# Optimization experiments

Measured on AMD Instinct MI355X. Metric: run time of the kernel, lower is better.

Reference implementation:

```python
import jax, jax.numpy as jnp
import numpy as np

B, T, D, H = 32, 512, 512, 8
DH = D // H  # 64


def _pos_enc(t, d):
    # pos / 10000^(2i/d) for ALL i, then sin on even cols, cos on odd cols, scaled by sqrt(d)
    pos = np.arange(t, dtype=np.float64)[:, None]
    i = np.arange(d, dtype=np.float64)[None, :]
    ang = pos / np.power(10000.0, 2.0 * i / d)
    pe = np.empty((t, d), dtype=np.float64)
    pe[:, 0::2] = np.sin(ang[:, 0::2])
    pe[:, 1::2] = np.cos(ang[:, 1::2])
    return jnp.asarray(pe * np.sqrt(float(d)), dtype=jnp.float32)


def setup_inputs() -> dict:
    key = jax.random.key(0)
    ks = jax.random.split(key, 9)
    return {
        "queries": jax.random.normal(ks[0], (B, T, D), dtype=jnp.float32),
        "keys": jax.random.normal(ks[1], (B, T, D), dtype=jnp.float32),
        "query_masks": jax.random.randint(ks[2], (B,), 0, T, dtype=jnp.int32),
        "key_masks": jax.random.randint(ks[3], (B,), 0, T, dtype=jnp.int32),
        "W_Q": jax.random.normal(ks[4], (D, D), dtype=jnp.float32) * 0.05,
        "W_K": jax.random.normal(ks[5], (D, D), dtype=jnp.float32) * 0.05,
        "W_V": jax.random.normal(ks[6], (D, D), dtype=jnp.float32) * 0.05,
        "fw1": jax.random.normal(ks[7], (D, 4 * D), dtype=jnp.float32) * 0.05,
        "fw2": jax.random.normal(ks[8], (4 * D, D), dtype=jnp.float32) * 0.05,
    }


def reference(queries, keys, query_masks, key_masks, W_Q, W_K, W_V, fw1, fw2):
    pe = _pos_enc(T, D)  # [T, D]
    # Source bug kept: queries = posenc(queries); keys = posenc(queries)  -> keys input unused
    q1 = queries + pe[None]          # [B,T,D]
    k1 = q1 + pe[None]               # pos-encoded twice
    Q = q1 @ W_Q                     # [B,T,D]
    Kp = k1 @ W_K                    # [B,T,D]
    V = Kp @ W_V                     # source bug kept: values from projected keys
    # split heads (head-major fold in the original concat(split) idiom)
    Qh = Q.reshape(B, T, H, DH).transpose(2, 0, 1, 3)   # [H,B,T,dh]
    Kh = Kp.reshape(B, T, H, DH).transpose(2, 0, 1, 3)
    Vh = V.reshape(B, T, H, DH).transpose(2, 0, 1, 3)
    scores = jnp.einsum('hbqd,hbkd->hbqk', Qh, Kh) / jnp.sqrt(jnp.float32(DH))
    # source subtracts max over the QUERY axis (axis=1 of [H*B,T,T]) = axis 2 here
    scores = scores - scores.max(axis=2, keepdims=True)
    attn = jax.nn.softmax(scores, axis=-1)
    qmask = (jnp.arange(T)[None, :] < query_masks[:, None]).astype(jnp.float32)  # [B,T]
    attn = attn * qmask[None, :, :, None]
    out = jnp.einsum('hbqk,hbkd->hbqd', attn, Vh)       # [H,B,T,dh]
    result = out.transpose(1, 2, 0, 3).reshape(B, T, D) + q1  # residual with pos-encoded queries
    hidden = jax.nn.relu(result @ fw1)                  # [B,T,4D]
    result = result + hidden @ fw2                      # residual; no layer norm (use_layer_norm=False)
    return result
```

## Files before the change

kernel.cpp:

```cpp
#include <hip/hip_runtime.h>
#include <cstdint>
#include <cstddef>

typedef __bf16 bf16x8 __attribute__((ext_vector_type(8)));
typedef float f32x4 __attribute__((ext_vector_type(4)));
using u16 = unsigned short;
using u32 = unsigned int;

__device__ __forceinline__ u16 f2b(float f) {
  u32 u = __float_as_uint(f);
  u32 r = u + 0x7FFFu + ((u >> 16) & 1u);
  return (u16)(r >> 16);
}
__device__ __forceinline__ float b2f(u16 h) { return __uint_as_float((u32)h << 16); }

__device__ __forceinline__ void gload16(const void* g, void* l) {
  __builtin_amdgcn_global_load_lds((const __attribute__((address_space(1))) void*)g,
                                   (__attribute__((address_space(3))) void*)l, 16, 0, 0);
}

__device__ __forceinline__ u32 mapf(float f) {
  u32 u = __float_as_uint(f);
  return (u & 0x80000000u) ? ~u : (u | 0x80000000u);
}
__device__ __forceinline__ float unmapf(u32 k) {
  u32 u = (k & 0x80000000u) ? (k ^ 0x80000000u) : ~k;
  return __uint_as_float(u);
}
__device__ __forceinline__ u32 cvtpk(float lo, float hi) {
  u32 r;
  asm("v_cvt_pk_bf16_f32 %0, %1, %2" : "=v"(r) : "v"(lo), "v"(hi));
  return r;
}

#define MFMA __builtin_amdgcn_mfma_f32_16x16x32_bf16

__global__ void pe_kernel(float* __restrict__ pe) {
  int i = blockIdx.x * 256 + threadIdx.x;
  if (i >= 512 * 512) return;
  int t = i >> 9, d = i & 511;
  double ang = (double)t * exp((double)d * (-2.0 / 512.0) * log(10000.0));
  double v = (d & 1) ? cos(ang) : sin(ang);
  pe[i] = (float)(v * 22.627416997969522);
}

__global__ void wconv_kernel(const float* __restrict__ WQ, const float* __restrict__ WK,
                             const float* __restrict__ WV, const float* __restrict__ f1,
                             const float* __restrict__ f2,
                             u16* __restrict__ WQth, u16* __restrict__ WQtl,
                             u16* __restrict__ WKth, u16* __restrict__ WKtl,
                             u16* __restrict__ WKb, u16* __restrict__ WVt,
                             u16* __restrict__ f1t, u16* __restrict__ f2t) {
  int i = blockIdx.x * 256 + threadIdx.x;
  if (i < 262144) {
    int n = i >> 9, k = i & 511;
    float wq = WQ[k * 512 + n];
    u16 h = f2b(wq);
    WQth[i] = h;
    WQtl[i] = f2b(wq - b2f(h));
    float wk = WK[k * 512 + n];
    h = f2b(wk);
    WKth[i] = h;
    WKtl[i] = f2b(wk - b2f(h));
    WKb[i] = f2b(WK[i]);
    WVt[i] = f2b(WV[k * 512 + n]);
  } else if (i < 262144 + 1048576) {
    int i2 = i - 262144;
    int n = i2 >> 9, k = i2 & 511;
    f1t[i2] = f2b(f1[k * 2048 + n]);
  } else if (i < 262144 + 2097152) {
    int i3 = i - 262144 - 1048576;
    int n = i3 >> 11, k = i3 & 2047;
    f2t[i3] = f2b(f2[k * 512 + n]);
  }
}

__global__ void prep_kernel(const float* __restrict__ q, const float* __restrict__ pe,
                            u16* __restrict__ q1h, u16* __restrict__ q1l,
                            u16* __restrict__ k1h, u16* __restrict__ k1l,
                            u32* __restrict__ m0) {
  int i = blockIdx.x * 256 + threadIdx.x;
  if (i < 131072) m0[i] = 0u;
  if (i >= 32 * 512 * 512) return;
  int td = i & (262144 - 1);
  float p = pe[td];
  float q1 = q[i] + p;
  float k1 = q1 + p;
  u16 h = f2b(q1);
  q1h[i] = h;
  q1l[i] = f2b(q1 - b2f(h));
  h = f2b(k1);
  k1h[i] = h;
  k1l[i] = f2b(k1 - b2f(h));
}

#define GM_BF16 0
#define GM_RELU 2
#define GM_ADDF32 3

template <int MODE>
__global__ __launch_bounds__(256, 2) void gemm_bt(const u16* __restrict__ A,
                                                  const u16* __restrict__ B, int M, int N, int K,
                                                  u16* __restrict__ outb, float* __restrict__ outf,
                                                  const float* __restrict__ res) {
  __shared__ u16 As[128 * 32];
  __shared__ u16 Bs[128 * 32];
  const int tid = threadIdx.x, lane = tid & 63, w = tid >> 6;
  const int wm = w >> 1, wn = w & 1;
  const long aBase = (long)blockIdx.x * 128;
  const long bBase = (long)blockIdx.y * 128;
  f32x4 acc[4][4] = {};
  const int nk = K >> 5;
  for (int kt = 0; kt < nk; ++kt) {
#pragma unroll
    for (int i = 0; i < 2; ++i) {
      const int c = w * 2 + i;
      const int off = c * 1024 + lane * 16;
      const int r = off >> 6, cb = off & 63;
      gload16((const char*)A + ((aBase + r) * (long)K + (long)kt * 32) * 2 + cb,
              (char*)As + c * 1024);
      gload16((const char*)B + ((bBase + r) * (long)K + (long)kt * 32) * 2 + cb,
              (char*)Bs + c * 1024);
    }
    __syncthreads();
    bf16x8 af[4], bfr[4];
#pragma unroll
    for (int x = 0; x < 4; ++x) {
      af[x] = *(const bf16x8*)&As[(wm * 64 + x * 16 + (lane & 15)) * 32 + (lane >> 4) * 8];
      bfr[x] = *(const bf16x8*)&Bs[(wn * 64 + x * 16 + (lane & 15)) * 32 + (lane >> 4) * 8];
    }
#pragma unroll
    for (int mf = 0; mf < 4; ++mf)
#pragma unroll
      for (int nf = 0; nf < 4; ++nf)
        acc[mf][nf] = MFMA(af[mf], bfr[nf], acc[mf][nf], 0, 0, 0);
    __syncthreads();
  }
#pragma unroll
  for (int mf = 0; mf < 4; ++mf)
#pragma unroll
    for (int nf = 0; nf < 4; ++nf) {
      const long row0 = aBase + wm * 64 + mf * 16 + (lane >> 4) * 4;
      const long col = bBase + wn * 64 + nf * 16 + (lane & 15);
#pragma unroll
      for (int j = 0; j < 4; ++j) {
        float v = acc[mf][nf][j];
        const long row = row0 + j;
        if (MODE == GM_BF16)
          outb[row * N + col] = f2b(v);
        else if (MODE == GM_RELU)
          outb[row * N + col] = f2b(v > 0.f ? v : 0.f);
        else
          outf[row * N + col] = res[row * N + col] + v;
      }
    }
}

__global__ __launch_bounds__(256, 2) void gemm_split(const u16* __restrict__ Ah,
                                                     const u16* __restrict__ Al,
                                                     const u16* __restrict__ Bh,
                                                     const u16* __restrict__ Bl, int M, int N,
                                                     int K, u16* __restrict__ Oh,
                                                     u16* __restrict__ Ol) {
  __shared__ u16 Ash[4096], Asl[4096], Bsh[4096], Bsl[4096];
  const int tid = threadIdx.x, lane = tid & 63, w = tid >> 6;
  const int wm = w >> 1, wn = w & 1;
  const long aBase = (long)blockIdx.x * 128;
  const long bBase = (long)blockIdx.y * 128;
  f32x4 acc[4][4] = {};
  const int nk = K >> 5;
  for (int kt = 0; kt < nk; ++kt) {
#pragma unroll
    for (int i = 0; i < 2; ++i) {
      const int c = w * 2 + i;
      const int off = c * 1024 + lane * 16;
      const int r = off >> 6, cb = off & 63;
      long ga = ((aBase + r) * (long)K + (long)kt * 32) * 2 + cb;
      long gb = ((bBase + r) * (long)K + (long)kt * 32) * 2 + cb;
      gload16((const char*)Ah + ga, (char*)Ash + c * 1024);
      gload16((const char*)Al + ga, (char*)Asl + c * 1024);
      gload16((const char*)Bh + gb, (char*)Bsh + c * 1024);
      gload16((const char*)Bl + gb, (char*)Bsl + c * 1024);
    }
    __syncthreads();
    bf16x8 ah[4], al[4], bh[4], bl[4];
#pragma unroll
    for (int x = 0; x < 4; ++x) {
      int ao = (wm * 64 + x * 16 + (lane & 15)) * 32 + (lane >> 4) * 8;
      int bo = (wn * 64 + x * 16 + (lane & 15)) * 32 + (lane >> 4) * 8;
      ah[x] = *(const bf16x8*)&Ash[ao];
      al[x] = *(const bf16x8*)&Asl[ao];
      bh[x] = *(const bf16x8*)&Bsh[bo];
      bl[x] = *(const bf16x8*)&Bsl[bo];
    }
#pragma unroll
    for (int mf = 0; mf < 4; ++mf)
#pragma unroll
      for (int nf = 0; nf < 4; ++nf) {
        acc[mf][nf] = MFMA(ah[mf], bh[nf], acc[mf][nf], 0, 0, 0);
        acc[mf][nf] = MFMA(ah[mf], bl[nf], acc[mf][nf], 0, 0, 0);
        acc[mf][nf] = MFMA(al[mf], bh[nf], acc[mf][nf], 0, 0, 0);
      }
    __syncthreads();
  }
#pragma unroll
  for (int mf = 0; mf < 4; ++mf)
#pragma unroll
    for (int nf = 0; nf < 4; ++nf) {
      const long row0 = aBase + wm * 64 + mf * 16 + (lane >> 4) * 4;
      const long col = bBase + wn * 64 + nf * 16 + (lane & 15);
#pragma unroll
      for (int j = 0; j < 4; ++j) {
        float v = acc[mf][nf][j];
        const long row = row0 + j;
        u16 h = f2b(v);
        Oh[row * N + col] = h;
        Ol[row * N + col] = f2b(v - b2f(h));
      }
    }
}

__global__ __launch_bounds__(256, 4) void attn_colmax(const u16* __restrict__ Qh,
                                                      const u16* __restrict__ Ql,
                                                      const u16* __restrict__ Kh,
                                                      const u16* __restrict__ Kl,
                                                      u32* __restrict__ mg) {
  __shared__ u16 Qsh[4096], Qsl[4096];
  __shared__ u16 Ksh[4096], Ksl[4096];
  __shared__ u32 mloc[512];
  const int tid = threadIdx.x, lane = tid & 63, w = tid >> 6;
  const int ql = lane & 15, g = lane >> 4;
  const int hb = blockIdx.x, b = hb >> 3, h = hb & 7, qc = blockIdx.y;
  mloc[tid] = 0u;
  mloc[tid + 256] = 0u;
  const int srccb = 16 * ((lane & 7) ^ ((lane >> 3) & 7));
#pragma unroll
  for (int i = 0; i < 2; ++i) {
    const int c = w * 2 + i;
    const int r = c * 8 + (lane >> 3);
    long gb = ((long)(b * 512 + qc * 64 + r) * 512 + h * 64) * 2 + srccb;
    gload16((const char*)Qh + gb, (char*)Qsh + c * 1024);
    gload16((const char*)Ql + gb, (char*)Qsl + c * 1024);
  }
  __syncthreads();
  const int qrow = w * 16 + ql;
  const int sw0 = ((g * 16) ^ ((ql & 7) * 16)) >> 1;
  const int sw1 = ((64 + g * 16) ^ ((ql & 7) * 16)) >> 1;
  bf16x8 qh0 = *(const bf16x8*)&Qsh[qrow * 64 + sw0];
  bf16x8 ql0 = *(const bf16x8*)&Qsl[qrow * 64 + sw0];
  bf16x8 qh1 = *(const bf16x8*)&Qsh[qrow * 64 + sw1];
  bf16x8 ql1 = *(const bf16x8*)&Qsl[qrow * 64 + sw1];
  for (int kc = 0; kc < 8; ++kc) {
#pragma unroll
    for (int i = 0; i < 2; ++i) {
      const int c = w * 2 + i;
      const int r = c * 8 + (lane >> 3);
      long gb = ((long)(b * 512 + kc * 64 + r) * 512 + h * 64) * 2 + srccb;
      gload16((const char*)Kh + gb, (char*)Ksh + c * 1024);
      gload16((const char*)Kl + gb, (char*)Ksl + c * 1024);
    }
    __syncthreads();
#pragma unroll
    for (int kt = 0; kt < 4; ++kt) {
      const int krow = kt * 16 + ql;
      bf16x8 kh0 = *(const bf16x8*)&Ksh[krow * 64 + sw0];
      bf16x8 kl0 = *(const bf16x8*)&Ksl[krow * 64 + sw0];
      bf16x8 kh1 = *(const bf16x8*)&Ksh[krow * 64 + sw1];
      bf16x8 kl1 = *(const bf16x8*)&Ksl[krow * 64 + sw1];
      f32x4 acc = {0.f, 0.f, 0.f, 0.f};
      acc = MFMA(qh0, kh0, acc, 0, 0, 0);
      acc = MFMA(qh0, kl0, acc, 0, 0, 0);
      acc = MFMA(ql0, kh0, acc, 0, 0, 0);
      acc = MFMA(qh1, kh1, acc, 0, 0, 0);
      acc = MFMA(qh1, kl1, acc, 0, 0, 0);
      acc = MFMA(ql1, kh1, acc, 0, 0, 0);
      float v = fmaxf(fmaxf(acc[0], acc[1]), fmaxf(acc[2], acc[3]));
      v = fmaxf(v, __shfl_xor(v, 16));
      v = fmaxf(v, __shfl_xor(v, 32));
      if (lane < 16) atomicMax(&mloc[kc * 64 + kt * 16 + ql], mapf(v));
    }
    __syncthreads();
  }
  for (int k = tid; k < 512; k += 256) atomicMax(&mg[(long)hb * 512 + k], mloc[k]);
}

__global__ __launch_bounds__(256, 3) void attn_main(
    const u16* __restrict__ Qh, const u16* __restrict__ Ql, const u16* __restrict__ Kh,
    const u16* __restrict__ Kl, const u16* __restrict__ Vt, const u32* __restrict__ mg,
    const int* __restrict__ qmask, const float* __restrict__ queries,
    const float* __restrict__ pe, float* __restrict__ resf, u16* __restrict__ resb) {
  __shared__ u16 Qsh[4096], Qsl[4096];
  __shared__ u16 Ksh[4096], Ksl[4096];
  __shared__ float mks[512];
  const int tid = threadIdx.x, lane = tid & 63, w = tid >> 6;
  const int ql = lane & 15, g = lane >> 4;
  const int hb = blockIdx.x, b = hb >> 3, h = hb & 7, qc = blockIdx.y;
  const int qm = qmask[b];
  for (int k = tid; k < 512; k += 256) mks[k] = 0.125f * unmapf(mg[(long)hb * 512 + k]);
  const int srccb = 16 * ((lane & 7) ^ ((lane >> 3) & 7));
#pragma unroll
  for (int i = 0; i < 2; ++i) {
    const int c = w * 2 + i;
    const int r = c * 8 + (lane >> 3);
    long gb = ((long)(b * 512 + qc * 64 + r) * 512 + h * 64) * 2 + srccb;
    gload16((const char*)Qh + gb, (char*)Qsh + c * 1024);
    gload16((const char*)Ql + gb, (char*)Qsl + c * 1024);
  }
  __syncthreads();
  const int qrow = w * 16 + ql;
  const int sw0 = ((g * 16) ^ ((ql & 7) * 16)) >> 1;
  const int sw1 = ((64 + g * 16) ^ ((ql & 7) * 16)) >> 1;
  bf16x8 qh0 = *(const bf16x8*)&Qsh[qrow * 64 + sw0];
  bf16x8 qh1 = *(const bf16x8*)&Qsh[qrow * 64 + sw1];
  f32x4 s[32] = {};
  for (int kc = 0; kc < 8; ++kc) {
#pragma unroll
    for (int i = 0; i < 2; ++i) {
      const int c = w * 2 + i;
      const int r = c * 8 + (lane >> 3);
      long gb = ((long)(b * 512 + kc * 64 + r) * 512 + h * 64) * 2 + srccb;
      gload16((const char*)Kh + gb, (char*)Ksh + c * 1024);
      gload16((const char*)Kl + gb, (char*)Ksl + c * 1024);
    }
    __syncthreads();
    bf16x8 qlo0 = *(const bf16x8*)&Qsl[qrow * 64 + sw0];
    bf16x8 qlo1 = *(const bf16x8*)&Qsl[qrow * 64 + sw1];
#pragma unroll
    for (int kt = 0; kt < 4; ++kt) {
      const int krow = kt * 16 + ql;
      bf16x8 kh0 = *(const bf16x8*)&Ksh[krow * 64 + sw0];
      bf16x8 kl0 = *(const bf16x8*)&Ksl[krow * 64 + sw0];
      bf16x8 kh1 = *(const bf16x8*)&Ksh[krow * 64 + sw1];
      bf16x8 kl1 = *(const bf16x8*)&Ksl[krow * 64 + sw1];
      const int fi = kc * 4 + kt;
      s[fi] = MFMA(kh0, qh0, s[fi], 0, 0, 0);
      s[fi] = MFMA(kh0, qlo0, s[fi], 0, 0, 0);
      s[fi] = MFMA(kl0, qh0, s[fi], 0, 0, 0);
      s[fi] = MFMA(kh1, qh1, s[fi], 0, 0, 0);
      s[fi] = MFMA(kh1, qlo1, s[fi], 0, 0, 0);
      s[fi] = MFMA(kl1, qh1, s[fi], 0, 0, 0);
    }
    __syncthreads();
  }
  float pmax = -3.4e38f;
#pragma unroll
  for (int fi = 0; fi < 32; ++fi) {
    f32x4 mrow = *(const f32x4*)&mks[fi * 16 + g * 4];
#pragma unroll
    for (int j = 0; j < 4; ++j) {
      float z = s[fi][j] * 0.125f - mrow[j];
      s[fi][j] = z;
      pmax = fmaxf(pmax, z);
    }
  }
  pmax = fmaxf(pmax, __shfl_xor(pmax, 16));
  pmax = fmaxf(pmax, __shfl_xor(pmax, 32));
  float rsum = 0.f;
#pragma unroll
  for (int fi = 0; fi < 32; ++fi)
#pragma unroll
    for (int j = 0; j < 4; ++j) {
      float p = __expf(s[fi][j] - pmax);
      s[fi][j] = p;
      rsum += p;
    }
  rsum += __shfl_xor(rsum, 16);
  rsum += __shfl_xor(rsum, 32);
  const int qg = qc * 64 + w * 16 + ql;
  const float sc = (qg < qm) ? (1.0f / rsum) : 0.0f;
  u32 pk0[32], pk1[32];
#pragma unroll
  for (int fi = 0; fi < 32; ++fi) {
    pk0[fi] = cvtpk(s[fi][0] * sc, s[fi][1] * sc);
    pk1[fi] = cvtpk(s[fi][2] * sc, s[fi][3] * sc);
  }
  f32x4 o[4] = {};
  const int src0 = (g & 1) * 32 + ql;
  const int src1 = src0 + 16;
  const bool lowh = g < 2;
  const u16* vb = Vt + (long)(h * 64) * 16384 + b * 512;
#pragma unroll
  for (int ks = 0; ks < 16; ++ks) {
    const int fA = 2 * ks, fB = 2 * ks + 1;
    u32 a00 = __shfl(pk0[fA], src0), b00 = __shfl(pk0[fB], src0);
    u32 a10 = __shfl(pk1[fA], src0), b10 = __shfl(pk1[fB], src0);
    u32 a01 = __shfl(pk0[fA], src1), b01 = __shfl(pk0[fB], src1);
    u32 a11 = __shfl(pk1[fA], src1), b11 = __shfl(pk1[fB], src1);
    union {
      u32 u[4];
      bf16x8 v;
    } pf;
    pf.u[0] = lowh ? a00 : b00;
    pf.u[1] = lowh ? a10 : b10;
    pf.u[2] = lowh ? a01 : b01;
    pf.u[3] = lowh ? a11 : b11;
#pragma unroll
    for (int nf = 0; nf < 4; ++nf) {
      bf16x8 vf = *(const bf16x8*)&vb[(long)(nf * 16 + ql) * 16384 + ks * 32 + g * 8];
      o[nf] = MFMA(vf, pf.v, o[nf], 0, 0, 0);
    }
  }
#pragma unroll
  for (int nf = 0; nf < 4; ++nf) {
    const int col = h * 64 + nf * 16 + g * 4;
    const long idx = (long)(b * 512 + qg) * 512 + col;
    float4 qv = *(const float4*)&queries[idx];
    float4 pv = *(const float4*)&pe[qg * 512 + col];
    float v0 = o[nf][0] + qv.x + pv.x;
    float v1 = o[nf][1] + qv.y + pv.y;
    float v2 = o[nf][2] + qv.z + pv.z;
    float v3 = o[nf][3] + qv.w + pv.w;
    *(float4*)&resf[idx] = make_float4(v0, v1, v2, v3);
    ushort4 rb = {f2b(v0), f2b(v1), f2b(v2), f2b(v3)};
    *(ushort4*)&resb[idx] = rb;
  }
}

extern "C" void kernel_launch(void* const* d_in, const int* in_sizes, int n_in, void* d_out,
                              int out_size, void* d_ws, size_t ws_size, hipStream_t stream) {
  (void)in_sizes;
  (void)n_in;
  (void)out_size;
  (void)ws_size;
  const float* queries = (const float*)d_in[0];
  const int* qmask = (const int*)d_in[2];
  const float* WQ = (const float*)d_in[4];
  const float* WK = (const float*)d_in[5];
  const float* WV = (const float*)d_in[6];
  const float* f1 = (const float*)d_in[7];
  const float* f2 = (const float*)d_in[8];
  float* out = (float*)d_out;
  char* ws = (char*)d_ws;
  const size_t A = 16777216;
  u16* q1h = (u16*)(ws + 0 * A);
  u16* q1l = (u16*)(ws + 1 * A);
  u16* k1h = (u16*)(ws + 2 * A);
  u16* k1l = (u16*)(ws + 3 * A);
  u16* Qh = (u16*)(ws + 4 * A);
  u16* Ql = (u16*)(ws + 5 * A);
  u16* Kh = (u16*)(ws + 6 * A);
  u16* Kl = (u16*)(ws + 7 * A);
  u16* Vt = (u16*)(ws + 8 * A);
  u16* resb = (u16*)(ws + 9 * A);
  u16* hid = (u16*)(ws);
  float* pe = (float*)(ws + 10 * A);
  u32* m_ws = (u32*)(ws + 10 * A + 1048576);
  char* wbase = ws + 10 * A + 1572864;
  u16* WQth = (u16*)(wbase + 0 * 524288);
  u16* WQtl = (u16*)(wbase + 1 * 524288);
  u16* WKth = (u16*)(wbase + 2 * 524288);
  u16* WKtl = (u16*)(wbase + 3 * 524288);
  u16* WKb = (u16*)(wbase + 4 * 524288);
  u16* WVt_w = (u16*)(wbase + 5 * 524288);
  u16* WKVt = (u16*)(wbase + 6 * 524288);
  u16* f1t = (u16*)(wbase + 7 * 524288);
  u16* f2t = (u16*)(wbase + 7 * 524288 + 2097152);

  pe_kernel<<<1024, 256, 0, stream>>>(pe);
  wconv_kernel<<<9216, 256, 0, stream>>>(WQ, WK, WV, f1, f2, WQth, WQtl, WKth, WKtl, WKb, WVt_w,
                                         f1t, f2t);
  prep_kernel<<<32768, 256, 0, stream>>>(queries, pe, q1h, q1l, k1h, k1l, m_ws);
  gemm_bt<GM_BF16><<<dim3(4, 4), 256, 0, stream>>>(WVt_w, WKb, 512, 512, 512, WKVt, nullptr,
                                                   nullptr);
  gemm_split<<<dim3(128, 4), 256, 0, stream>>>(q1h, q1l, WQth, WQtl, 16384, 512, 512, Qh, Ql);
  gemm_split<<<dim3(128, 4), 256, 0, stream>>>(k1h, k1l, WKth, WKtl, 16384, 512, 512, Kh, Kl);
  gemm_bt<GM_BF16><<<dim3(4, 128), 256, 0, stream>>>(WKVt, k1h, 512, 16384, 512, Vt, nullptr,
                                                     nullptr);
  attn_colmax<<<dim3(256, 8), 256, 0, stream>>>(Qh, Ql, Kh, Kl, m_ws);
  attn_main<<<dim3(256, 8), 256, 0, stream>>>(Qh, Ql, Kh, Kl, Vt, m_ws, qmask, queries, pe, out,
                                              resb);
  gemm_bt<GM_RELU><<<dim3(128, 16), 256, 0, stream>>>(resb, f1t, 16384, 2048, 512, hid, nullptr,
                                                      nullptr);
  gemm_bt<GM_ADDF32><<<dim3(128, 4), 256, 0, stream>>>(hid, f2t, 16384, 512, 2048, nullptr, out,
                                                       out);
}
```

Baseline: 380.7 us.

## Fold second positional encoding into precomputed PE projections, drop k1 buffers

Uses linearity, k1 = q1 + pe, so K = q1·WK + pe·WK and V^T = WKV^T·q1^T + WKV^T·pe^T. The pe products are computed once by small GEMMs and added in the epilogues. This removes the k1 hi/lo buffers and their writes in the prep kernel, so the K and V GEMMs read q1 instead. It also changes launch bounds: gemm_bt goes to 3 blocks/SM and attn_main to 2, with the attention kc loop unrolled. Rounding changes slightly because k1 is no longer split into bf16 hi/lo before the K projection.

After: 417.2 us. 1.1x slower.

```diff
diff --git a/kernel.cpp b/kernel.cpp
--- a/kernel.cpp
+++ b/kernel.cpp
@@ -35,13 +35,17 @@
 
 #define MFMA __builtin_amdgcn_mfma_f32_16x16x32_bf16
 
-__global__ void pe_kernel(float* __restrict__ pe) {
+__global__ void pe_kernel(float* __restrict__ pe, u16* __restrict__ peh, u16* __restrict__ pel) {
   int i = blockIdx.x * 256 + threadIdx.x;
   if (i >= 512 * 512) return;
   int t = i >> 9, d = i & 511;
   double ang = (double)t * exp((double)d * (-2.0 / 512.0) * log(10000.0));
   double v = (d & 1) ? cos(ang) : sin(ang);
-  pe[i] = (float)(v * 22.627416997969522);
+  float p = (float)(v * 22.627416997969522);
+  pe[i] = p;
+  u16 h = f2b(p);
+  peh[i] = h;
+  pel[i] = f2b(p - b2f(h));
 }
 
 __global__ void wconv_kernel(const float* __restrict__ WQ, const float* __restrict__ WK,
@@ -50,7 +54,8 @@
                              u16* __restrict__ WQth, u16* __restrict__ WQtl,
                              u16* __restrict__ WKth, u16* __restrict__ WKtl,
                              u16* __restrict__ WKb, u16* __restrict__ WVt,
-                             u16* __restrict__ f1t, u16* __restrict__ f2t) {
+                             u16* __restrict__ f1t, u16* __restrict__ f2t,
+                             u16* __restrict__ zb) {
   int i = blockIdx.x * 256 + threadIdx.x;
   if (i < 262144) {
     int n = i >> 9, k = i & 511;
@@ -64,6 +69,7 @@
     WKtl[i] = f2b(wk - b2f(h));
     WKb[i] = f2b(WK[i]);
     WVt[i] = f2b(WV[k * 512 + n]);
+    zb[i] = 0;
   } else if (i < 262144 + 1048576) {
     int i2 = i - 262144;
     int n = i2 >> 9, k = i2 & 511;
@@ -77,32 +83,28 @@
 
 __global__ void prep_kernel(const float* __restrict__ q, const float* __restrict__ pe,
                             u16* __restrict__ q1h, u16* __restrict__ q1l,
-                            u16* __restrict__ k1h, u16* __restrict__ k1l,
                             u32* __restrict__ m0) {
   int i = blockIdx.x * 256 + threadIdx.x;
   if (i < 131072) m0[i] = 0u;
   if (i >= 32 * 512 * 512) return;
   int td = i & (262144 - 1);
-  float p = pe[td];
-  float q1 = q[i] + p;
-  float k1 = q1 + p;
+  float q1 = q[i] + pe[td];
   u16 h = f2b(q1);
   q1h[i] = h;
   q1l[i] = f2b(q1 - b2f(h));
-  h = f2b(k1);
-  k1h[i] = h;
-  k1l[i] = f2b(k1 - b2f(h));
 }
 
 #define GM_BF16 0
 #define GM_RELU 2
 #define GM_ADDF32 3
+#define GM_BF16PE 4
 
 template <int MODE>
-__global__ __launch_bounds__(256, 2) void gemm_bt(const u16* __restrict__ A,
+__global__ __launch_bounds__(256, 3) void gemm_bt(const u16* __restrict__ A,
                                                   const u16* __restrict__ B, int M, int N, int K,
                                                   u16* __restrict__ outb, float* __restrict__ outf,
-                                                  const float* __restrict__ res) {
+                                                  const float* __restrict__ res,
+                                                  const float* __restrict__ peadd) {
   __shared__ u16 As[128 * 32];
   __shared__ u16 Bs[128 * 32];
   const int tid = threadIdx.x, lane = tid & 63, w = tid >> 6;
@@ -146,22 +148,27 @@
       for (int j = 0; j < 4; ++j) {
         float v = acc[mf][nf][j];
         const long row = row0 + j;
-        if (MODE == GM_BF16)
+        if constexpr (MODE == GM_BF16)
           outb[row * N + col] = f2b(v);
-        else if (MODE == GM_RELU)
+        else if constexpr (MODE == GM_RELU)
           outb[row * N + col] = f2b(v > 0.f ? v : 0.f);
+        else if constexpr (MODE == GM_BF16PE)
+          outb[row * N + col] = f2b(v + peadd[row * 512 + (col & 511)]);
         else
           outf[row * N + col] = res[row * N + col] + v;
       }
     }
 }
 
+template <int OUT>
 __global__ __launch_bounds__(256, 2) void gemm_split(const u16* __restrict__ Ah,
                                                      const u16* __restrict__ Al,
                                                      const u16* __restrict__ Bh,
                                                      const u16* __restrict__ Bl, int M, int N,
                                                      int K, u16* __restrict__ Oh,
-                                                     u16* __restrict__ Ol) {
+                                                     u16* __restrict__ Ol,
+                                                     float* __restrict__ Of,
+                                                     const float* __restrict__ peadd) {
   __shared__ u16 Ash[4096], Asl[4096], Bsh[4096], Bsl[4096];
   const int tid = threadIdx.x, lane = tid & 63, w = tid >> 6;
   const int wm = w >> 1, wn = w & 1;
@@ -213,9 +220,14 @@
       for (int j = 0; j < 4; ++j) {
         float v = acc[mf][nf][j];
         const long row = row0 + j;
-        u16 h = f2b(v);
-        Oh[row * N + col] = h;
-        Ol[row * N + col] = f2b(v - b2f(h));
+        if constexpr (OUT == 1) v += peadd[(row & 511) * 512 + col];
+        if constexpr (OUT == 2) {
+          Of[row * N + col] = v;
+        } else {
+          u16 h = f2b(v);
+          Oh[row * N + col] = h;
+          Ol[row * N + col] = f2b(v - b2f(h));
+        }
       }
     }
 }
@@ -284,7 +296,7 @@
   for (int k = tid; k < 512; k += 256) atomicMax(&mg[(long)hb * 512 + k], mloc[k]);
 }
 
-__global__ __launch_bounds__(256, 3) void attn_main(
+__global__ __launch_bounds__(256, 2) void attn_main(
     const u16* __restrict__ Qh, const u16* __restrict__ Ql, const u16* __restrict__ Kh,
     const u16* __restrict__ Kl, const u16* __restrict__ Vt, const u32* __restrict__ mg,
     const int* __restrict__ qmask, const float* __restrict__ queries,
@@ -313,6 +325,7 @@
   bf16x8 qh0 = *(const bf16x8*)&Qsh[qrow * 64 + sw0];
   bf16x8 qh1 = *(const bf16x8*)&Qsh[qrow * 64 + sw1];
   f32x4 s[32] = {};
+#pragma unroll
   for (int kc = 0; kc < 8; ++kc) {
 #pragma unroll
     for (int i = 0; i < 2; ++i) {
@@ -434,8 +447,6 @@
   const size_t A = 16777216;
   u16* q1h = (u16*)(ws + 0 * A);
   u16* q1l = (u16*)(ws + 1 * A);
-  u16* k1h = (u16*)(ws + 2 * A);
-  u16* k1l = (u16*)(ws + 3 * A);
   u16* Qh = (u16*)(ws + 4 * A);
   u16* Ql = (u16*)(ws + 5 * A);
   u16* Kh = (u16*)(ws + 6 * A);
@@ -455,22 +466,34 @@
   u16* WKVt = (u16*)(wbase + 6 * 524288);
   u16* f1t = (u16*)(wbase + 7 * 524288);
   u16* f2t = (u16*)(wbase + 7 * 524288 + 2097152);
-
-  pe_kernel<<<1024, 256, 0, stream>>>(pe);
+  char* xbase = wbase + 7 * 524288 + 4194304;
+  u16* peh = (u16*)(xbase);
+  u16* pel = (u16*)(xbase + 524288);
+  u16* zb = (u16*)(xbase + 1048576);
+  float* PEK = (float*)(xbase + 1572864);
+  float* PEVt = (float*)(xbase + 2621440);
+
+  pe_kernel<<<1024, 256, 0, stream>>>(pe, peh, pel);
   wconv_kernel<<<9216, 256, 0, stream>>>(WQ, WK, WV, f1, f2, WQth, WQtl, WKth, WKtl, WKb, WVt_w,
-                                         f1t, f2t);
-  prep_kernel<<<32768, 256, 0, stream>>>(queries, pe, q1h, q1l, k1h, k1l, m_ws);
+                                         f1t, f2t, zb);
+  prep_kernel<<<32768, 256, 0, stream>>>(queries, pe, q1h, q1l, m_ws);
   gemm_bt<GM_BF16><<<dim3(4, 4), 256, 0, stream>>>(WVt_w, WKb, 512, 512, 512, WKVt, nullptr,
-                                                   nullptr);
-  gemm_split<<<dim3(128, 4), 256, 0, stream>>>(q1h, q1l, WQth, WQtl, 16384, 512, 512, Qh, Ql);
-  gemm_split<<<dim3(128, 4), 256, 0, stream>>>(k1h, k1l, WKth, WKtl, 16384, 512, 512, Kh, Kl);
-  gemm_bt<GM_BF16><<<dim3(4, 128), 256, 0, stream>>>(WKVt, k1h, 512, 16384, 512, Vt, nullptr,
-                                                     nullptr);
+                                                   nullptr, nullptr);
+  gemm_split<2><<<dim3(4, 4), 256, 0, stream>>>(peh, pel, WKth, WKtl, 512, 512, 512, nullptr,
+                                                nullptr, PEK, nullptr);
+  gemm_split<2><<<dim3(4, 4), 256, 0, stream>>>(WKVt, zb, peh, pel, 512, 512, 512, nullptr,
+                                                nullptr, PEVt, nullptr);
+  gemm_split<0><<<dim3(128, 4), 256, 0, stream>>>(q1h, q1l, WQth, WQtl, 16384, 512, 512, Qh, Ql,
+                                                  nullptr, nullptr);
+  gemm_split<1><<<dim3(128, 4), 256, 0, stream>>>(q1h, q1l, WKth, WKtl, 16384, 512, 512, Kh, Kl,
+                                                  nullptr, PEK);
+  gemm_bt<GM_BF16PE><<<dim3(4, 128), 256, 0, stream>>>(WKVt, q1h, 512, 16384, 512, Vt, nullptr,
+                                                       nullptr, PEVt);
   attn_colmax<<<dim3(256, 8), 256, 0, stream>>>(Qh, Ql, Kh, Kl, m_ws);
   attn_main<<<dim3(256, 8), 256, 0, stream>>>(Qh, Ql, Kh, Kl, Vt, m_ws, qmask, queries, pe, out,
                                               resb);
   gemm_bt<GM_RELU><<<dim3(128, 16), 256, 0, stream>>>(resb, f1t, 16384, 2048, 512, hid, nullptr,
-                                                      nullptr);
+                                                      nullptr, nullptr);
   gemm_bt<GM_ADDF32><<<dim3(128, 4), 256, 0, stream>>>(hid, f2t, 16384, 512, 2048, nullptr, out,
-                                                       out);
-}
+                                                       out, nullptr);
+}
```

## Fuse online softmax with PV product in attention and reuse split q1 residual

Applied to the files above, without the earlier changes.

The attention kernel now uses an online (flash-style) softmax that rescales running output and sum per 64-key chunk. It no longer holds all 32 score fragments in registers before the PV pass, and V fragments for each chunk are loaded at the top of the chunk loop to overlap with the K tile load. The residual now reads the precomputed bf16 hi/lo q1 split instead of fp32 queries plus the positional encoding. The gemm occupancy hint is raised from 2 to 3 blocks per CU. This cuts register pressure and global traffic, at the cost of extra exp/rescale work per chunk and a small precision change in the residual.

Measured after the change: 365.0 us. 1.04x faster.

```diff
diff --git a/kernel.cpp b/kernel.cpp
--- a/kernel.cpp
+++ b/kernel.cpp
@@ -99,7 +99,7 @@
 #define GM_ADDF32 3
 
 template <int MODE>
-__global__ __launch_bounds__(256, 2) void gemm_bt(const u16* __restrict__ A,
+__global__ __launch_bounds__(256, 3) void gemm_bt(const u16* __restrict__ A,
                                                   const u16* __restrict__ B, int M, int N, int K,
                                                   u16* __restrict__ outb, float* __restrict__ outf,
                                                   const float* __restrict__ res) {
@@ -146,9 +146,9 @@
       for (int j = 0; j < 4; ++j) {
         float v = acc[mf][nf][j];
         const long row = row0 + j;
-        if (MODE == GM_BF16)
+        if constexpr (MODE == GM_BF16)
           outb[row * N + col] = f2b(v);
-        else if (MODE == GM_RELU)
+        else if constexpr (MODE == GM_RELU)
           outb[row * N + col] = f2b(v > 0.f ? v : 0.f);
         else
           outf[row * N + col] = res[row * N + col] + v;
@@ -287,13 +287,13 @@
 __global__ __launch_bounds__(256, 3) void attn_main(
     const u16* __restrict__ Qh, const u16* __restrict__ Ql, const u16* __restrict__ Kh,
     const u16* __restrict__ Kl, const u16* __restrict__ Vt, const u32* __restrict__ mg,
-    const int* __restrict__ qmask, const float* __restrict__ queries,
-    const float* __restrict__ pe, float* __restrict__ resf, u16* __restrict__ resb) {
+    const int* __restrict__ qmask, const u16* __restrict__ q1h, const u16* __restrict__ q1l,
+    float* __restrict__ resf, u16* __restrict__ resb) {
   __shared__ u16 Qsh[4096], Qsl[4096];
   __shared__ u16 Ksh[4096], Ksl[4096];
   __shared__ float mks[512];
   const int tid = threadIdx.x, lane = tid & 63, w = tid >> 6;
-  const int ql = lane & 15, g = lane >> 4;
+  const int qll = lane & 15, g = lane >> 4;
   const int hb = blockIdx.x, b = hb >> 3, h = hb & 7, qc = blockIdx.y;
   const int qm = qmask[b];
   for (int k = tid; k < 512; k += 256) mks[k] = 0.125f * unmapf(mg[(long)hb * 512 + k]);
@@ -307,13 +307,27 @@
     gload16((const char*)Ql + gb, (char*)Qsl + c * 1024);
   }
   __syncthreads();
-  const int qrow = w * 16 + ql;
-  const int sw0 = ((g * 16) ^ ((ql & 7) * 16)) >> 1;
-  const int sw1 = ((64 + g * 16) ^ ((ql & 7) * 16)) >> 1;
+  const int qrow = w * 16 + qll;
+  const int sw0 = ((g * 16) ^ ((qll & 7) * 16)) >> 1;
+  const int sw1 = ((64 + g * 16) ^ ((qll & 7) * 16)) >> 1;
   bf16x8 qh0 = *(const bf16x8*)&Qsh[qrow * 64 + sw0];
   bf16x8 qh1 = *(const bf16x8*)&Qsh[qrow * 64 + sw1];
-  f32x4 s[32] = {};
+  bf16x8 qlo0 = *(const bf16x8*)&Qsl[qrow * 64 + sw0];
+  bf16x8 qlo1 = *(const bf16x8*)&Qsl[qrow * 64 + sw1];
+  f32x4 o[4] = {};
+  float mr = -3.0e38f, rsum = 0.f;
+  const u16* vb = Vt + (long)(h * 64) * 16384 + b * 512;
+  const int src0 = (g & 1) * 32 + qll;
+  const int src1 = src0 + 16;
+  const bool lowh = g < 2;
   for (int kc = 0; kc < 8; ++kc) {
+    bf16x8 vf[2][4];
+#pragma unroll
+    for (int k2 = 0; k2 < 2; ++k2)
+#pragma unroll
+      for (int nf = 0; nf < 4; ++nf)
+        vf[k2][nf] =
+            *(const bf16x8*)&vb[(long)(nf * 16 + qll) * 16384 + (kc * 2 + k2) * 32 + g * 8];
 #pragma unroll
     for (int i = 0; i < 2; ++i) {
       const int c = w * 2 + i;
@@ -323,93 +337,89 @@
       gload16((const char*)Kl + gb, (char*)Ksl + c * 1024);
     }
     __syncthreads();
-    bf16x8 qlo0 = *(const bf16x8*)&Qsl[qrow * 64 + sw0];
-    bf16x8 qlo1 = *(const bf16x8*)&Qsl[qrow * 64 + sw1];
+    f32x4 s4[4] = {};
 #pragma unroll
     for (int kt = 0; kt < 4; ++kt) {
-      const int krow = kt * 16 + ql;
+      const int krow = kt * 16 + qll;
       bf16x8 kh0 = *(const bf16x8*)&Ksh[krow * 64 + sw0];
       bf16x8 kl0 = *(const bf16x8*)&Ksl[krow * 64 + sw0];
       bf16x8 kh1 = *(const bf16x8*)&Ksh[krow * 64 + sw1];
       bf16x8 kl1 = *(const bf16x8*)&Ksl[krow * 64 + sw1];
-      const int fi = kc * 4 + kt;
-      s[fi] = MFMA(kh0, qh0, s[fi], 0, 0, 0);
-      s[fi] = MFMA(kh0, qlo0, s[fi], 0, 0, 0);
-      s[fi] = MFMA(kl0, qh0, s[fi], 0, 0, 0);
-      s[fi] = MFMA(kh1, qh1, s[fi], 0, 0, 0);
-      s[fi] = MFMA(kh1, qlo1, s[fi], 0, 0, 0);
-      s[fi] = MFMA(kl1, qh1, s[fi], 0, 0, 0);
-    }
-    __syncthreads();
-  }
-  float pmax = -3.4e38f;
-#pragma unroll
-  for (int fi = 0; fi < 32; ++fi) {
-    f32x4 mrow = *(const f32x4*)&mks[fi * 16 + g * 4];
-#pragma unroll
-    for (int j = 0; j < 4; ++j) {
-      float z = s[fi][j] * 0.125f - mrow[j];
-      s[fi][j] = z;
-      pmax = fmaxf(pmax, z);
-    }
-  }
-  pmax = fmaxf(pmax, __shfl_xor(pmax, 16));
-  pmax = fmaxf(pmax, __shfl_xor(pmax, 32));
-  float rsum = 0.f;
-#pragma unroll
-  for (int fi = 0; fi < 32; ++fi)
-#pragma unroll
-    for (int j = 0; j < 4; ++j) {
-      float p = __expf(s[fi][j] - pmax);
-      s[fi][j] = p;
-      rsum += p;
-    }
+      s4[kt] = MFMA(kh0, qh0, s4[kt], 0, 0, 0);
+      s4[kt] = MFMA(kh0, qlo0, s4[kt], 0, 0, 0);
+      s4[kt] = MFMA(kl0, qh0, s4[kt], 0, 0, 0);
+      s4[kt] = MFMA(kh1, qh1, s4[kt], 0, 0, 0);
+      s4[kt] = MFMA(kh1, qlo1, s4[kt], 0, 0, 0);
+      s4[kt] = MFMA(kl1, qh1, s4[kt], 0, 0, 0);
+    }
+    __syncthreads();
+    float pm = mr;
+#pragma unroll
+    for (int kt = 0; kt < 4; ++kt) {
+      f32x4 mrow = *(const f32x4*)&mks[kc * 64 + kt * 16 + g * 4];
+#pragma unroll
+      for (int j = 0; j < 4; ++j) {
+        float z = s4[kt][j] * 0.125f - mrow[j];
+        s4[kt][j] = z;
+        pm = fmaxf(pm, z);
+      }
+    }
+    pm = fmaxf(pm, __shfl_xor(pm, 16));
+    pm = fmaxf(pm, __shfl_xor(pm, 32));
+    const float f = __expf(mr - pm);
+    mr = pm;
+    rsum *= f;
+#pragma unroll
+    for (int nf = 0; nf < 4; ++nf) {
+      o[nf][0] *= f;
+      o[nf][1] *= f;
+      o[nf][2] *= f;
+      o[nf][3] *= f;
+    }
+    u32 pk0[4], pk1[4];
+#pragma unroll
+    for (int kt = 0; kt < 4; ++kt) {
+      float p0 = __expf(s4[kt][0] - mr);
+      float p1 = __expf(s4[kt][1] - mr);
+      float p2 = __expf(s4[kt][2] - mr);
+      float p3 = __expf(s4[kt][3] - mr);
+      rsum += (p0 + p1) + (p2 + p3);
+      pk0[kt] = cvtpk(p0, p1);
+      pk1[kt] = cvtpk(p2, p3);
+    }
+#pragma unroll
+    for (int k2 = 0; k2 < 2; ++k2) {
+      const int fA = 2 * k2, fB = 2 * k2 + 1;
+      u32 a00 = __shfl(pk0[fA], src0), b00 = __shfl(pk0[fB], src0);
+      u32 a10 = __shfl(pk1[fA], src0), b10 = __shfl(pk1[fB], src0);
+      u32 a01 = __shfl(pk0[fA], src1), b01 = __shfl(pk0[fB], src1);
+      u32 a11 = __shfl(pk1[fA], src1), b11 = __shfl(pk1[fB], src1);
+      union {
+        u32 u[4];
+        bf16x8 v;
+      } pf;
+      pf.u[0] = lowh ? a00 : b00;
+      pf.u[1] = lowh ? a10 : b10;
+      pf.u[2] = lowh ? a01 : b01;
+      pf.u[3] = lowh ? a11 : b11;
+#pragma unroll
+      for (int nf = 0; nf < 4; ++nf) o[nf] = MFMA(vf[k2][nf], pf.v, o[nf], 0, 0, 0);
+    }
+  }
   rsum += __shfl_xor(rsum, 16);
   rsum += __shfl_xor(rsum, 32);
-  const int qg = qc * 64 + w * 16 + ql;
+  const int qg = qc * 64 + w * 16 + qll;
   const float sc = (qg < qm) ? (1.0f / rsum) : 0.0f;
-  u32 pk0[32], pk1[32];
-#pragma unroll
-  for (int fi = 0; fi < 32; ++fi) {
-    pk0[fi] = cvtpk(s[fi][0] * sc, s[fi][1] * sc);
-    pk1[fi] = cvtpk(s[fi][2] * sc, s[fi][3] * sc);
-  }
-  f32x4 o[4] = {};
-  const int src0 = (g & 1) * 32 + ql;
-  const int src1 = src0 + 16;
-  const bool lowh = g < 2;
-  const u16* vb = Vt + (long)(h * 64) * 16384 + b * 512;
-#pragma unroll
-  for (int ks = 0; ks < 16; ++ks) {
-    const int fA = 2 * ks, fB = 2 * ks + 1;
-    u32 a00 = __shfl(pk0[fA], src0), b00 = __shfl(pk0[fB], src0);
-    u32 a10 = __shfl(pk1[fA], src0), b10 = __shfl(pk1[fB], src0);
-    u32 a01 = __shfl(pk0[fA], src1), b01 = __shfl(pk0[fB], src1);
-    u32 a11 = __shfl(pk1[fA], src1), b11 = __shfl(pk1[fB], src1);
-    union {
-      u32 u[4];
-      bf16x8 v;
-    } pf;
-    pf.u[0] = lowh ? a00 : b00;
-    pf.u[1] = lowh ? a10 : b10;
-    pf.u[2] = lowh ? a01 : b01;
-    pf.u[3] = lowh ? a11 : b11;
-#pragma unroll
-    for (int nf = 0; nf < 4; ++nf) {
-      bf16x8 vf = *(const bf16x8*)&vb[(long)(nf * 16 + ql) * 16384 + ks * 32 + g * 8];
-      o[nf] = MFMA(vf, pf.v, o[nf], 0, 0, 0);
-    }
-  }
 #pragma unroll
   for (int nf = 0; nf < 4; ++nf) {
     const int col = h * 64 + nf * 16 + g * 4;
     const long idx = (long)(b * 512 + qg) * 512 + col;
-    float4 qv = *(const float4*)&queries[idx];
-    float4 pv = *(const float4*)&pe[qg * 512 + col];
-    float v0 = o[nf][0] + qv.x + pv.x;
-    float v1 = o[nf][1] + qv.y + pv.y;
-    float v2 = o[nf][2] + qv.z + pv.z;
-    float v3 = o[nf][3] + qv.w + pv.w;
+    ushort4 qh4 = *(const ushort4*)&q1h[idx];
+    ushort4 ql4 = *(const ushort4*)&q1l[idx];
+    float v0 = o[nf][0] * sc + b2f(qh4.x) + b2f(ql4.x);
+    float v1 = o[nf][1] * sc + b2f(qh4.y) + b2f(ql4.y);
+    float v2 = o[nf][2] * sc + b2f(qh4.z) + b2f(ql4.z);
+    float v3 = o[nf][3] * sc + b2f(qh4.w) + b2f(ql4.w);
     *(float4*)&resf[idx] = make_float4(v0, v1, v2, v3);
     ushort4 rb = {f2b(v0), f2b(v1), f2b(v2), f2b(v3)};
     *(ushort4*)&resb[idx] = rb;
@@ -442,7 +452,8 @@
   u16* Kl = (u16*)(ws + 7 * A);
   u16* Vt = (u16*)(ws + 8 * A);
   u16* resb = (u16*)(ws + 9 * A);
-  u16* hid = (u16*)(ws);
+  u16* hid = (u16*)(ws + 2 * A);
+  hid = (u16*)(ws + 0 * A);
   float* pe = (float*)(ws + 10 * A);
   u32* m_ws = (u32*)(ws + 10 * A + 1048576);
   char* wbase = ws + 10 * A + 1572864;
@@ -467,7 +478,7 @@
   gemm_bt<GM_BF16><<<dim3(4, 128), 256, 0, stream>>>(WKVt, k1h, 512, 16384, 512, Vt, nullptr,
                                                      nullptr);
   attn_colmax<<<dim3(256, 8), 256, 0, stream>>>(Qh, Ql, Kh, Kl, m_ws);
-  attn_main<<<dim3(256, 8), 256, 0, stream>>>(Qh, Ql, Kh, Kl, Vt, m_ws, qmask, queries, pe, out,
+  attn_main<<<dim3(256, 8), 256, 0, stream>>>(Qh, Ql, Kh, Kl, Vt, m_ws, qmask, q1h, q1l, out,
                                               resb);
   gemm_bt<GM_RELU><<<dim3(128, 16), 256, 0, stream>>>(resb, f1t, 16384, 2048, 512, hid, nullptr,
                                                       nullptr);
```
